# Performance work log

Measured on AMD Instinct MI355X. Metric: run time of the kernel, lower is better.

## Reference

```python
import jax, jax.numpy as jnp
import numpy as np

B, S, D_MODEL, H = 8, 1024, 512, 8
DEPTH = D_MODEL // H


def setup_inputs() -> dict:
    key = jax.random.key(0)
    ks = jax.random.split(key, 12)
    q = jax.random.normal(ks[0], (B, S, D_MODEL), dtype=jnp.float32)
    k = jax.random.normal(ks[1], (B, S, D_MODEL), dtype=jnp.float32)
    v = jax.random.normal(ks[2], (B, S, D_MODEL), dtype=jnp.float32)
    # mask: 1.0 = masked-out key position (multiplied by -1e9 inside), 0.0 = attend
    mask = jax.random.bernoulli(ks[3], 0.1, (B, 1, 1, S)).astype(jnp.float32)
    adj = jax.random.bernoulli(ks[4], 0.05, (B, S, S)).astype(jnp.float32)
    dist = jax.random.uniform(ks[5], (B, S, S), dtype=jnp.float32)
    scale = 1.0 / np.sqrt(D_MODEL)
    Wq = jax.random.normal(ks[6], (D_MODEL, D_MODEL), dtype=jnp.float32) * scale
    Wk = jax.random.normal(ks[7], (D_MODEL, D_MODEL), dtype=jnp.float32) * scale
    Wv = jax.random.normal(ks[8], (D_MODEL, D_MODEL), dtype=jnp.float32) * scale
    Wo = jax.random.normal(ks[9], (D_MODEL, D_MODEL), dtype=jnp.float32) * scale
    bq = jnp.zeros((D_MODEL,), jnp.float32)
    bk = jnp.zeros((D_MODEL,), jnp.float32)
    bv = jnp.zeros((D_MODEL,), jnp.float32)
    bo = jnp.zeros((D_MODEL,), jnp.float32)
    return {"q": q, "k": k, "v": v, "mask": mask, "adj": adj, "dist": dist,
            "Wq": Wq, "bq": bq, "Wk": Wk, "bk": bk, "Wv": Wv, "bv": bv,
            "Wo": Wo, "bo": bo}


def _split_heads(x):
    # (B, S, D) -> (B, H, S, depth)
    b, s, _ = x.shape
    return x.reshape(b, s, H, DEPTH).transpose(0, 2, 1, 3)


def reference(q, k, v, mask, adj, dist, Wq, bq, Wk, bk, Wv, bv, Wo, bo):
    b = q.shape[0]
    qh = _split_heads(q @ Wq + bq)  # (B,H,Sq,depth)
    kh = _split_heads(k @ Wk + bk)
    vh = _split_heads(v @ Wv + bv)

    neg_mask = mask * -1e9  # (B,1,1,S)
    dk = jnp.asarray(kh.shape[-1], jnp.float32)
    logits = jnp.einsum("bhqd,bhkd->bhqk", qh, kh) / jnp.sqrt(dk) + neg_mask
    attn = jax.nn.softmax(logits, axis=-1)  # (B,H,Sq,Sk)

    attn = attn * adj[:, None, :, :]
    dist_sm = jax.nn.softmax(dist[:, None, :, :] + neg_mask, axis=-1)  # 'original'
    attn = attn * dist_sm

    ctx = jnp.einsum("bhqk,bhkd->bhqd", attn, vh)
    concat = ctx.transpose(0, 2, 1, 3).reshape(b, -1, D_MODEL)
    out = concat @ Wo + bo
    return out, attn
```

## Files before the change

kernel.cpp:

```cpp
#include <hip/hip_runtime.h>
#include <hip/hip_bf16.h>

#define BB 8
#define SS 1024
#define DM 512
#define HH 8
#define BM 128
#define BN 128
#define BK 32
#define LD 40

typedef __bf16 bf16x8 __attribute__((ext_vector_type(8)));
typedef __bf16 bf16x4 __attribute__((ext_vector_type(4)));
typedef float f32x4 __attribute__((ext_vector_type(4)));

__device__ __forceinline__ f32x4 mfma16(bf16x8 a, bf16x8 b, f32x4 c) {
    return __builtin_amdgcn_mfma_f32_16x16x32_bf16(a, b, c, 0, 0, 0);
}

__global__ __launch_bounds__(256) void wconv(
    const float* __restrict__ W0, const float* __restrict__ W1,
    const float* __restrict__ W2, const float* __restrict__ W3,
    __bf16* __restrict__ th, __bf16* __restrict__ tl)
{
    const float* W = blockIdx.z == 0 ? W0 : blockIdx.z == 1 ? W1
                   : blockIdx.z == 2 ? W2 : W3;
    __bf16* oh = th + (size_t)blockIdx.z * 512 * 512;
    __bf16* ol = tl + (size_t)blockIdx.z * 512 * 512;
    __shared__ float T[64][65];
    const int k0 = blockIdx.x * 64, n0 = blockIdx.y * 64;
    const int r = threadIdx.x >> 4, c4 = (threadIdx.x & 15) * 4;
    #pragma unroll
    for (int p = 0; p < 4; ++p) {
        float4 v = *(const float4*)(W + (size_t)(k0 + p * 16 + r) * 512 + n0 + c4);
        T[p * 16 + r][c4 + 0] = v.x; T[p * 16 + r][c4 + 1] = v.y;
        T[p * 16 + r][c4 + 2] = v.z; T[p * 16 + r][c4 + 3] = v.w;
    }
    __syncthreads();
    #pragma unroll
    for (int p = 0; p < 4; ++p) {
        int n = n0 + p * 16 + r;
        bf16x4 h4, l4;
        #pragma unroll
        for (int j = 0; j < 4; ++j) {
            float x = T[c4 + j][p * 16 + r];
            __bf16 h = (__bf16)x;
            h4[j] = h; l4[j] = (__bf16)(x - (float)h);
        }
        *(bf16x4*)(oh + (size_t)n * 512 + k0 + c4) = h4;
        *(bf16x4*)(ol + (size_t)n * 512 + k0 + c4) = l4;
    }
}

template<int MODE>
__global__ __launch_bounds__(256, 3) void gemm_tile(
    const float* __restrict__ Aq, const float* __restrict__ Ak,
    const float* __restrict__ Av,
    const __bf16* __restrict__ Ahig, const __bf16* __restrict__ Alog,
    const __bf16* __restrict__ Wth, const __bf16* __restrict__ Wtl,
    const float* __restrict__ bq, const float* __restrict__ bk,
    const float* __restrict__ bv,
    float* __restrict__ Cf, __bf16* __restrict__ qo, __bf16* __restrict__ ko,
    __bf16* __restrict__ vo)
{
    __shared__ __align__(16) __bf16 Ah[BM][LD];
    __shared__ __align__(16) __bf16 Al[(MODE == 1 ? BM : 1)][LD];
    __shared__ __align__(16) __bf16 Bh[BN][LD];
    __shared__ __align__(16) __bf16 Bl[BN][LD];

    const int tid = threadIdx.x;
    const int w = tid >> 6, lane = tid & 63, l15 = lane & 15, lg = lane >> 4;
    const int wm = w >> 1, wn = w & 1;
    const int bx = blockIdx.x;
    const int z  = MODE == 0 ? (bx >> 2) : 3;
    const int n0 = MODE == 0 ? (bx & 3) * BN : bx * BN;
    const int m0 = blockIdx.y * BM;

    const float* Afp = (MODE == 0) ? (z == 0 ? Aq : z == 1 ? Ak : Av) : nullptr;
    const __bf16* wh = Wth + (size_t)z * 512 * 512;
    const __bf16* wl = Wtl + (size_t)z * 512 * 512;

    f32x4 acc[4][4];
    #pragma unroll
    for (int i = 0; i < 4; ++i)
        #pragma unroll
        for (int j = 0; j < 4; ++j) acc[i][j] = (f32x4){0.f, 0.f, 0.f, 0.f};

    for (int k0 = 0; k0 < 512; k0 += BK) {
        __syncthreads();
        if (MODE == 0) {
            const int row = tid >> 3, c = (tid & 7) * 4;
            #pragma unroll
            for (int p = 0; p < 4; ++p) {
                int rr = row + p * 32;
                f32x4 a = *(const f32x4*)(Afp + (size_t)(m0 + rr) * 512 + k0 + c);
                bf16x4 h4;
                #pragma unroll
                for (int j = 0; j < 4; ++j) h4[j] = (__bf16)a[j];
                *(bf16x4*)&Ah[rr][c] = h4;
            }
        } else {
            const int row = tid >> 2, c = (tid & 3) * 8;
            #pragma unroll
            for (int p = 0; p < 2; ++p) {
                int rr = row + p * 64;
                *(bf16x8*)&Ah[rr][c] =
                    *(const bf16x8*)(Ahig + (size_t)(m0 + rr) * 512 + k0 + c);
                *(bf16x8*)&Al[rr][c] =
                    *(const bf16x8*)(Alog + (size_t)(m0 + rr) * 512 + k0 + c);
            }
        }
        {
            const int row = tid >> 2, c = (tid & 3) * 8;
            #pragma unroll
            for (int p = 0; p < 2; ++p) {
                int rr = row + p * 64;
                *(bf16x8*)&Bh[rr][c] =
                    *(const bf16x8*)(wh + (size_t)(n0 + rr) * 512 + k0 + c);
                *(bf16x8*)&Bl[rr][c] =
                    *(const bf16x8*)(wl + (size_t)(n0 + rr) * 512 + k0 + c);
            }
        }
        __syncthreads();

        bf16x8 afh[4], afl[4];
        #pragma unroll
        for (int mt = 0; mt < 4; ++mt) {
            afh[mt] = *(const bf16x8*)&Ah[wm * 64 + mt * 16 + l15][lg * 8];
            if (MODE == 1)
                afl[mt] = *(const bf16x8*)&Al[wm * 64 + mt * 16 + l15][lg * 8];
        }
        #pragma unroll
        for (int nt = 0; nt < 4; ++nt) {
            bf16x8 bfh = *(const bf16x8*)&Bh[wn * 64 + nt * 16 + l15][lg * 8];
            bf16x8 bfl = *(const bf16x8*)&Bl[wn * 64 + nt * 16 + l15][lg * 8];
            #pragma unroll
            for (int mt = 0; mt < 4; ++mt) {
                acc[mt][nt] = mfma16(afh[mt], bfh, acc[mt][nt]);
                acc[mt][nt] = mfma16(afh[mt], bfl, acc[mt][nt]);
                if (MODE == 1)
                    acc[mt][nt] = mfma16(afl[mt], bfh, acc[mt][nt]);
            }
        }
    }

    const float* bias = (MODE == 1) ? bq : (z == 0 ? bq : z == 1 ? bk : bv);
    #pragma unroll
    for (int nt = 0; nt < 4; ++nt) {
        const int n = n0 + wn * 64 + nt * 16 + l15;
        const float bz = bias[n];
        #pragma unroll
        for (int mt = 0; mt < 4; ++mt) {
            if (MODE == 0 && z == 2) {
                bf16x4 v4;
                int mbase = m0 + wm * 64 + mt * 16 + lg * 4;
                #pragma unroll
                for (int rr = 0; rr < 4; ++rr)
                    v4[rr] = (__bf16)(acc[mt][nt][rr] + bz);
                int bb = mbase >> 10, s = mbase & 1023, h = n >> 6, d = n & 63;
                *(bf16x4*)(vo + ((size_t)(bb * HH + h) * 64 + d) * SS + s) = v4;
            } else {
                #pragma unroll
                for (int rr = 0; rr < 4; ++rr) {
                    int m = m0 + wm * 64 + mt * 16 + lg * 4 + rr;
                    float v = acc[mt][nt][rr] + bz;
                    if (MODE == 1) {
                        Cf[(size_t)m * 512 + n] = v;
                    } else {
                        int bb = m >> 10, s = m & 1023, h = n >> 6, d = n & 63;
                        __bf16* outp = z == 0 ? qo : ko;
                        outp[((size_t)(bb * HH + h) * SS + s) * 64 + d] = (__bf16)v;
                    }
                }
            }
        }
    }
}

__global__ __launch_bounds__(256) void gprep(
    const float* __restrict__ mask, const float* __restrict__ adj,
    const float* __restrict__ dist,
    __bf16* __restrict__ Gg, float* __restrict__ rowILg)
{
    const int w = threadIdx.x >> 6, lane = threadIdx.x & 63;
    const int row = blockIdx.x * 4 + w;
    const int b = row >> 10;
    const size_t drow = (size_t)row * SS;
    const float L2E = 1.44269504f;
    const float* mrow = mask + (size_t)b * SS;
    float sm = 0.f;
    #pragma unroll
    for (int j = 0; j < 4; ++j) {
        int c = lane * 4 + j * 256;
        f32x4 d4 = *(const f32x4*)(dist + drow + c);
        f32x4 a4 = *(const f32x4*)(adj + drow + c);
        f32x4 m4 = *(const f32x4*)(mrow + c);
        bf16x4 g4;
        #pragma unroll
        for (int r = 0; r < 4; ++r) {
            float e = exp2f(fmaf(m4[r], -1e9f * L2E, fmaf(d4[r], L2E, -L2E)));
            sm += e;
            g4[r] = (__bf16)(a4[r] * e);
        }
        *(bf16x4*)(Gg + drow + c) = g4;
    }
    #pragma unroll
    for (int off = 1; off <= 32; off <<= 1)
        sm += __shfl_xor(sm, off, 64);
    if (lane == 0) rowILg[row] = 1.0f / sm;
}

__global__ __launch_bounds__(512, 4) void attn10(
    const __bf16* __restrict__ qh_, const __bf16* __restrict__ kh,
    const __bf16* __restrict__ vt,
    const float* __restrict__ mask, const __bf16* __restrict__ Gg,
    const float* __restrict__ rowILg,
    float* __restrict__ attn_out, __bf16* __restrict__ chi, __bf16* __restrict__ clo)
{
    __shared__ float nmb[1024];
    __shared__ __align__(16) __bf16 P[32][1024];
    __shared__ __align__(16) __bf16 KV[64][64];
    __shared__ float redl[8][16];

    const int tid = threadIdx.x;
    const int w = tid >> 6, lane = tid & 63, l15 = lane & 15, lg = lane >> 4;
    const int bid = blockIdx.x;
    const int h = bid & 7;
    const int b = (bid >> 3) & 7;
    const int q0 = (bid >> 6) * 32;
    const float L2E = 1.44269504f;
    const float c1 = 0.125f * L2E;

    char* Pb = (char*)P;
    char* KVb = (char*)KV;
    const int srow = tid >> 3;
    const int scol = (tid & 7) * 8;
    const int sdst = srow * 128 + ((scol * 2) ^ ((srow & 7) << 4));

    #pragma unroll
    for (int i = 0; i < 2; ++i) {
        int c = tid + 512 * i;
        nmb[c] = fmaf(mask[(size_t)b * SS + c], -1e9f * L2E, -16.0f * L2E);
    }

    const size_t hb = ((size_t)(b * HH + h)) * SS * 64;
    const int qsub = w >> 2, ktw = w & 3;
    bf16x8 qf0 = *(const bf16x8*)(qh_ + hb + (size_t)(q0 + qsub * 16 + l15) * 64 + lg * 8);
    bf16x8 qf1 = *(const bf16x8*)(qh_ + hb + (size_t)(q0 + qsub * 16 + l15) * 64 + 32 + lg * 8);

    const int krow = ktw * 16 + l15;
    const int kswz = (krow & 7) << 4;
    const int prow = qsub * 16 + l15;
    const int pswz = (prow & 7) << 4;

    const __bf16* kcp = kh + hb + (size_t)srow * 64 + scol;
    bf16x8 kvreg = *(const bf16x8*)kcp;
    float lac = 0.f;
    for (int c = 0; c < 16; ++c) {
        __syncthreads();
        *(bf16x8*)(KVb + sdst) = kvreg;
        __syncthreads();
        if (c + 1 < 16)
            kvreg = *(const bf16x8*)(kcp + (size_t)(c + 1) * 4096);
        bf16x8 k0v = *(const bf16x8*)(KVb + krow * 128 + ((lg * 16) ^ kswz));
        bf16x8 k1v = *(const bf16x8*)(KVb + krow * 128 + ((64 + lg * 16) ^ kswz));
        f32x4 acc = {0.f, 0.f, 0.f, 0.f};
        acc = mfma16(k0v, qf0, acc);
        acc = mfma16(k1v, qf1, acc);
        const int key4 = c * 64 + ktw * 16 + lg * 4;
        f32x4 nb4 = *(const f32x4*)&nmb[key4];
        float e0 = exp2f(fmaf(acc[0], c1, nb4[0]));
        float e1 = exp2f(fmaf(acc[1], c1, nb4[1]));
        float e2 = exp2f(fmaf(acc[2], c1, nb4[2]));
        float e3 = exp2f(fmaf(acc[3], c1, nb4[3]));
        lac += (e0 + e1) + (e2 + e3);
        bf16x4 pb;
        pb[0] = (__bf16)e0; pb[1] = (__bf16)e1;
        pb[2] = (__bf16)e2; pb[3] = (__bf16)e3;
        *(bf16x4*)(Pb + prow * 2048 + ((key4 * 2) ^ pswz)) = pb;
    }
    #pragma unroll
    for (int off = 16; off <= 32; off <<= 1)
        lac += __shfl_xor(lac, off, 64);
    if (lg == 0) redl[w][l15] = lac;
    __syncthreads();

    const float* rg = rowILg + (size_t)b * SS + q0;
    float* aoutb = attn_out + ((size_t)(b * HH + h)) * SS * SS;
    const __bf16* gb = Gg + ((size_t)b * SS + q0) * SS;
    #pragma unroll
    for (int r = 0; r < 4; ++r) {
        const int row = w * 4 + r;
        const int rs = (row >> 4) * 4;
        const float ltot = redl[rs][row & 15] + redl[rs + 1][row & 15]
                         + redl[rs + 2][row & 15] + redl[rs + 3][row & 15];
        const float coefR = rg[row] / ltot;
        const int rswz = (row & 7) << 4;
        float* ar = aoutb + (size_t)(q0 + row) * SS;
        const __bf16* gr = gb + (size_t)row * SS;
        #pragma unroll
        for (int j = 0; j < 4; ++j) {
            const int off = lane * 8 + j * 512;
            char* pp = Pb + row * 2048 + (off ^ rswz);
            bf16x4 e4 = *(const bf16x4*)pp;
            bf16x4 g4 = *(const bf16x4*)(gr + (off >> 1));
            f32x4 av;
            bf16x4 pb;
            #pragma unroll
            for (int r2 = 0; r2 < 4; ++r2) {
                float v = (float)e4[r2] * (float)g4[r2] * coefR;
                av[r2] = v;
                pb[r2] = (__bf16)v;
            }
            __builtin_nontemporal_store(av, (f32x4*)(ar + (off >> 1)));
            *(bf16x4*)pp = pb;
        }
    }

    const int dh = w & 3;
    const int vrow = dh * 16 + l15;
    const int vswz = (vrow & 7) << 4;
    f32x4 cacc = {0.f, 0.f, 0.f, 0.f};
    const __bf16* vcp = vt + ((size_t)(b * HH + h) * 64 + srow) * SS + scol;
    bf16x8 vreg = *(const bf16x8*)vcp;
    for (int c = 0; c < 16; ++c) {
        __syncthreads();
        *(bf16x8*)(KVb + sdst) = vreg;
        __syncthreads();
        if (c + 1 < 16)
            vreg = *(const bf16x8*)(vcp + (c + 1) * 64);
        #pragma unroll
        for (int ks = 0; ks < 2; ++ks) {
            bf16x8 pa = *(const bf16x8*)(Pb + prow * 2048
                          + ((c * 128 + ks * 64 + lg * 16) ^ pswz));
            bf16x8 vv = *(const bf16x8*)(KVb + vrow * 128 + ((ks * 64 + lg * 16) ^ vswz));
            cacc = mfma16(pa, vv, cacc);
        }
    }

    #pragma unroll
    for (int r = 0; r < 4; ++r) {
        const int row = qsub * 16 + lg * 4 + r;
        float x = cacc[r];
        __bf16 hv = (__bf16)x;
        size_t idx = ((size_t)b * SS + q0 + row) * DM + h * 64 + dh * 16 + l15;
        chi[idx] = hv;
        clo[idx] = (__bf16)(x - (float)hv);
    }
}

extern "C" void kernel_launch(void* const* d_in, const int* in_sizes, int n_in,
                              void* d_out, int out_size, void* d_ws, size_t ws_size,
                              hipStream_t stream) {
    const float* q    = (const float*)d_in[0];
    const float* k    = (const float*)d_in[1];
    const float* v    = (const float*)d_in[2];
    const float* mask = (const float*)d_in[3];
    const float* adj  = (const float*)d_in[4];
    const float* dist = (const float*)d_in[5];
    const float* Wq   = (const float*)d_in[6];
    const float* bq   = (const float*)d_in[7];
    const float* Wk   = (const float*)d_in[8];
    const float* bk   = (const float*)d_in[9];
    const float* Wv   = (const float*)d_in[10];
    const float* bv   = (const float*)d_in[11];
    const float* Wo   = (const float*)d_in[12];
    const float* bo   = (const float*)d_in[13];

    const size_t NT = (size_t)BB * SS * DM;
    const size_t WN = 512 * 512;
    const size_t NSS = (size_t)BB * SS * SS;
    __bf16* wth = (__bf16*)d_ws;
    __bf16* wtl = wth + 4 * WN;
    __bf16* qhb = wtl + 4 * WN;
    __bf16* khb = qhb + NT;
    __bf16* vtb = khb + NT;
    __bf16* chi = vtb + NT;
    __bf16* clo = chi + NT;
    __bf16* Gg  = clo + NT;
    float* rowILg = (float*)(Gg + NSS);

    float* outp = (float*)d_out;
    float* attn = outp + NT;

    wconv<<<dim3(8, 8, 4), 256, 0, stream>>>(Wq, Wk, Wv, Wo, wth, wtl);

    gprep<<<2048, 256, 0, stream>>>(mask, adj, dist, Gg, rowILg);

    gemm_tile<0><<<dim3(12, 64), 256, 0, stream>>>(
        q, k, v, nullptr, nullptr, wth, wtl, bq, bk, bv,
        nullptr, qhb, khb, vtb);

    attn10<<<2048, 512, 0, stream>>>(qhb, khb, vtb, mask, Gg, rowILg, attn, chi, clo);

    gemm_tile<1><<<dim3(4, 64), 256, 0, stream>>>(
        nullptr, nullptr, nullptr, chi, clo, wth, wtl, bo, nullptr, nullptr,
        outp, nullptr, nullptr, nullptr);
}
```

Baseline: 194.6 us.

## Double the attention query tile to 64 rows and double-buffer K/V staging

The attention kernel now runs 1024-thread blocks that each cover 64 query rows instead of 32, which halves the number of blocks and halves how often each K/V head tile is reloaded. The K and V staging buffers in LDS become double-buffered, so each chunk iteration needs one barrier instead of two and the next chunk's store overlaps the current compute. The cost is a much larger LDS footprint (the P buffer doubles), which likely limits the kernel to one block per CU. Larger blocks also make each barrier more expensive.

```diff
diff --git a/kernel.cpp b/kernel.cpp
--- a/kernel.cpp
+++ b/kernel.cpp
@@ -210,7 +210,7 @@
     if (lane == 0) rowILg[row] = 1.0f / sm;
 }
 
-__global__ __launch_bounds__(512, 4) void attn10(
+__global__ __launch_bounds__(1024, 4) void attn11(
     const __bf16* __restrict__ qh_, const __bf16* __restrict__ kh,
     const __bf16* __restrict__ vt,
     const float* __restrict__ mask, const __bf16* __restrict__ Gg,
@@ -218,30 +218,26 @@
     float* __restrict__ attn_out, __bf16* __restrict__ chi, __bf16* __restrict__ clo)
 {
     __shared__ float nmb[1024];
-    __shared__ __align__(16) __bf16 P[32][1024];
-    __shared__ __align__(16) __bf16 KV[64][64];
-    __shared__ float redl[8][16];
+    __shared__ __align__(16) __bf16 P[64][1024];
+    __shared__ __align__(16) __bf16 KV[2][64][64];
+    __shared__ float redl[16][16];
 
     const int tid = threadIdx.x;
     const int w = tid >> 6, lane = tid & 63, l15 = lane & 15, lg = lane >> 4;
     const int bid = blockIdx.x;
     const int h = bid & 7;
     const int b = (bid >> 3) & 7;
-    const int q0 = (bid >> 6) * 32;
+    const int q0 = (bid >> 6) * 64;
     const float L2E = 1.44269504f;
     const float c1 = 0.125f * L2E;
 
     char* Pb = (char*)P;
     char* KVb = (char*)KV;
-    const int srow = tid >> 3;
-    const int scol = (tid & 7) * 8;
+    const int srow = tid >> 4;
+    const int scol = (tid & 15) * 4;
     const int sdst = srow * 128 + ((scol * 2) ^ ((srow & 7) << 4));
 
-    #pragma unroll
-    for (int i = 0; i < 2; ++i) {
-        int c = tid + 512 * i;
-        nmb[c] = fmaf(mask[(size_t)b * SS + c], -1e9f * L2E, -16.0f * L2E);
-    }
+    nmb[tid] = fmaf(mask[(size_t)b * SS + tid], -1e9f * L2E, -16.0f * L2E);
 
     const size_t hb = ((size_t)(b * HH + h)) * SS * 64;
     const int qsub = w >> 2, ktw = w & 3;
@@ -254,16 +250,16 @@
     const int pswz = (prow & 7) << 4;
 
     const __bf16* kcp = kh + hb + (size_t)srow * 64 + scol;
-    bf16x8 kvreg = *(const bf16x8*)kcp;
+    bf16x4 kvreg = *(const bf16x4*)kcp;
+    *(bf16x4*)(KVb + sdst) = kvreg;
+    __syncthreads();
     float lac = 0.f;
     for (int c = 0; c < 16; ++c) {
-        __syncthreads();
-        *(bf16x8*)(KVb + sdst) = kvreg;
-        __syncthreads();
         if (c + 1 < 16)
-            kvreg = *(const bf16x8*)(kcp + (size_t)(c + 1) * 4096);
-        bf16x8 k0v = *(const bf16x8*)(KVb + krow * 128 + ((lg * 16) ^ kswz));
-        bf16x8 k1v = *(const bf16x8*)(KVb + krow * 128 + ((64 + lg * 16) ^ kswz));
+            kvreg = *(const bf16x4*)(kcp + (size_t)(c + 1) * 4096);
+        const char* kb = KVb + (c & 1) * 8192;
+        bf16x8 k0v = *(const bf16x8*)(kb + krow * 128 + ((lg * 16) ^ kswz));
+        bf16x8 k1v = *(const bf16x8*)(kb + krow * 128 + ((64 + lg * 16) ^ kswz));
         f32x4 acc = {0.f, 0.f, 0.f, 0.f};
         acc = mfma16(k0v, qf0, acc);
         acc = mfma16(k1v, qf1, acc);
@@ -278,6 +274,9 @@
         pb[0] = (__bf16)e0; pb[1] = (__bf16)e1;
         pb[2] = (__bf16)e2; pb[3] = (__bf16)e3;
         *(bf16x4*)(Pb + prow * 2048 + ((key4 * 2) ^ pswz)) = pb;
+        if (c + 1 < 16)
+            *(bf16x4*)(KVb + ((c + 1) & 1) * 8192 + sdst) = kvreg;
+        __syncthreads();
     }
     #pragma unroll
     for (int off = 16; off <= 32; off <<= 1)
@@ -322,20 +321,23 @@
     const int vswz = (vrow & 7) << 4;
     f32x4 cacc = {0.f, 0.f, 0.f, 0.f};
     const __bf16* vcp = vt + ((size_t)(b * HH + h) * 64 + srow) * SS + scol;
-    bf16x8 vreg = *(const bf16x8*)vcp;
+    bf16x4 vreg = *(const bf16x4*)vcp;
+    *(bf16x4*)(KVb + sdst) = vreg;
+    __syncthreads();
     for (int c = 0; c < 16; ++c) {
-        __syncthreads();
-        *(bf16x8*)(KVb + sdst) = vreg;
-        __syncthreads();
         if (c + 1 < 16)
-            vreg = *(const bf16x8*)(vcp + (c + 1) * 64);
+            vreg = *(const bf16x4*)(vcp + (c + 1) * 64);
+        const char* vbuf = KVb + (c & 1) * 8192;
         #pragma unroll
         for (int ks = 0; ks < 2; ++ks) {
             bf16x8 pa = *(const bf16x8*)(Pb + prow * 2048
                           + ((c * 128 + ks * 64 + lg * 16) ^ pswz));
-            bf16x8 vv = *(const bf16x8*)(KVb + vrow * 128 + ((ks * 64 + lg * 16) ^ vswz));
+            bf16x8 vv = *(const bf16x8*)(vbuf + vrow * 128 + ((ks * 64 + lg * 16) ^ vswz));
             cacc = mfma16(pa, vv, cacc);
         }
+        if (c + 1 < 16)
+            *(bf16x4*)(KVb + ((c + 1) & 1) * 8192 + sdst) = vreg;
+        __syncthreads();
     }
 
     #pragma unroll
@@ -391,7 +393,7 @@
         q, k, v, nullptr, nullptr, wth, wtl, bq, bk, bv,
         nullptr, qhb, khb, vtb);
 
-    attn10<<<2048, 512, 0, stream>>>(qhb, khb, vtb, mask, Gg, rowILg, attn, chi, clo);
+    attn11<<<1024, 1024, 0, stream>>>(qhb, khb, vtb, mask, Gg, rowILg, attn, chi, clo);
 
     gemm_tile<1><<<dim3(4, 64), 256, 0, stream>>>(
         nullptr, nullptr, nullptr, chi, clo, wth, wtl, bo, nullptr, nullptr,
```

New measurement: 206.6 us. 6.2% more time.
